# Kernel tuning notes

Hardware: AMD Instinct MI355X
Metric: run time of the kernel (lower is better)

## Reference

```python
import jax, jax.numpy as jnp
import numpy as np

N, K, D = 100000, 16, 128

def setup_inputs() -> dict:
    key = jax.random.key(0)
    k1, k2, k3, k4, k5 = jax.random.split(key, 5)
    s = 1.0 / np.sqrt(D)  # nn.Linear default init scale
    return {
        "h": jax.random.normal(k1, (N, D), dtype=jnp.float32),
        "nbr_idx": jax.random.randint(k2, (N, K), 0, N, dtype=jnp.int64),
        "nbr_w": jax.random.uniform(k3, (N, K), dtype=jnp.float32),
        "w_self": jax.random.uniform(k4, (D, D), minval=-s, maxval=s, dtype=jnp.float32),
        "w_nei": jax.random.uniform(k5, (D, D), minval=-s, maxval=s, dtype=jnp.float32),
        "ln_gamma": jnp.ones((D,), dtype=jnp.float32),
        "ln_beta": jnp.zeros((D,), dtype=jnp.float32),
    }

def layer_norm(x, gamma, beta, eps=1e-5):
    mu = jnp.mean(x, axis=-1, keepdims=True)
    var = jnp.mean(jnp.square(x - mu), axis=-1, keepdims=True)
    return (x - mu) * jax.lax.rsqrt(var + eps) * gamma + beta

def reference(h, nbr_idx, nbr_w, w_self, w_nei, ln_gamma, ln_beta):
    # gather neighbor features: [N, K, D]
    nei = h[nbr_idx]
    # weighted sum over neighbors -> [N, D]
    agg = jnp.einsum('nk,nkd->nd', nbr_w, nei)
    # dual linear (nn.Linear applies x @ W.T) + exact (erf) GELU
    out = jax.nn.gelu(h @ w_self.T + agg @ w_nei.T, approximate=False)
    # dropout is identity at inference; then LayerNorm
    return layer_norm(out, ln_gamma, ln_beta)
```

## Files before the change

kernel.cpp:

```cpp
#include <hip/hip_runtime.h>
#include <hip/hip_bf16.h>
#include <math.h>

#define DFEAT 128
#define KNBR  16
#define NPB   64

typedef __attribute__((ext_vector_type(8))) short short8;
typedef __attribute__((ext_vector_type(4))) float f32x4;
typedef __attribute__((ext_vector_type(2))) unsigned u32x2;
typedef __attribute__((ext_vector_type(4))) unsigned u32x4;

__device__ __forceinline__ unsigned short f2bf(float x) {
    union { float f; unsigned u; } v; v.f = x;
    unsigned r = v.u + 0x7FFFu + ((v.u >> 16) & 1u);
    return (unsigned short)(r >> 16);
}
__device__ __forceinline__ float bf2f(unsigned short u) {
    union { unsigned u; float f; } v; v.u = ((unsigned)u) << 16; return v.f;
}

__global__ __launch_bounds__(256)
void prep_kernel(const float* __restrict__ h,
                 const float* __restrict__ wself,
                 const float* __restrict__ wnei,
                 unsigned short* __restrict__ h16,
                 unsigned short* __restrict__ wcat,
                 unsigned char* __restrict__ h8i,
                 float* __restrict__ sc,
                 int ntot8) {
    const int t = blockIdx.x * 256 + threadIdx.x;
    if (t < 4096) {
        const int base = t * 8;
        const int j = base >> 8;
        const int d0 = base & 255;
        const float* src = (d0 < DFEAT) ? (wself + j * DFEAT + d0)
                                        : (wnei  + j * DFEAT + (d0 - DFEAT));
        f32x4 a = ((const f32x4*)src)[0], b = ((const f32x4*)src)[1];
        short8 o;
        o[0] = f2bf(a[0]); o[1] = f2bf(a[1]); o[2] = f2bf(a[2]); o[3] = f2bf(a[3]);
        o[4] = f2bf(b[0]); o[5] = f2bf(b[1]); o[6] = f2bf(b[2]); o[7] = f2bf(b[3]);
        *(short8*)(wcat + base) = o;
        return;
    }
    const long u = (long)t - 4096;
    if (u >= ntot8) return;
    f32x4 a = __builtin_nontemporal_load((const f32x4*)(h + u * 8));
    f32x4 b = __builtin_nontemporal_load((const f32x4*)(h + u * 8) + 1);
    short8 o;
    o[0] = f2bf(a[0]); o[1] = f2bf(a[1]); o[2] = f2bf(a[2]); o[3] = f2bf(a[3]);
    o[4] = f2bf(b[0]); o[5] = f2bf(b[1]); o[6] = f2bf(b[2]); o[7] = f2bf(b[3]);
    __builtin_nontemporal_store(o, (short8*)(h16 + u * 8));

    if (h8i) {
        float m = 0.f;
        #pragma unroll
        for (int d = 0; d < 4; ++d) { m = fmaxf(m, fabsf(a[d])); m = fmaxf(m, fabsf(b[d])); }
        #pragma unroll
        for (int mk = 1; mk < 16; mk <<= 1) m = fmaxf(m, __shfl_xor(m, mk, 64));
        const float inv = (m > 0.f) ? 127.f / m : 0.f;
        u32x2 q;
        q[0] = ((unsigned)((int)rintf(a[0] * inv) & 255))
             | ((unsigned)((int)rintf(a[1] * inv) & 255) << 8)
             | ((unsigned)((int)rintf(a[2] * inv) & 255) << 16)
             | ((unsigned)((int)rintf(a[3] * inv) & 255) << 24);
        q[1] = ((unsigned)((int)rintf(b[0] * inv) & 255))
             | ((unsigned)((int)rintf(b[1] * inv) & 255) << 8)
             | ((unsigned)((int)rintf(b[2] * inv) & 255) << 16)
             | ((unsigned)((int)rintf(b[3] * inv) & 255) << 24);
        __builtin_nontemporal_store(q, (u32x2*)(h8i + u * 8));
        if ((u & 15) == 0) sc[u >> 4] = m * (1.f / 127.f);
    }
}

template<int MODE>
__global__ __launch_bounds__(256, 4)
void sage_fused_kernel(const float* __restrict__ h,
                       const unsigned short* __restrict__ h16,
                       const unsigned char* __restrict__ h8i,
                       const float* __restrict__ sc,
                       const int* __restrict__ nbr32,
                       const float* __restrict__ nbrw,
                       const unsigned short* __restrict__ wcat,
                       const float* __restrict__ gamma,
                       const float* __restrict__ beta,
                       float* __restrict__ out,
                       int N) {
    __shared__ __align__(16) unsigned short xlds[NPB][256];

    const int tid = threadIdx.x;
    const int nb  = blockIdx.x * NPB;

    const bool idx64 = ((nbr32[1] | nbr32[3] | nbr32[5] | nbr32[7] |
                         nbr32[9] | nbr32[11] | nbr32[13] | nbr32[15]) == 0);

    const int l   = tid & 63;
    const int wvi = tid >> 6;

    if constexpr (MODE == 3) {
        const int q8  = l & 7;
        const int gb2 = l & 56;
        const int i0b = wvi * 16 + (l >> 3) * 2;

        #pragma unroll
        for (int r = 0; r < 2; ++r) {
            const int i = i0b + r;
            int n = nb + i; if (n >= N) n = N - 1;

            const int e0 = n * KNBR + q8;
            const int id0 = nbr32[idx64 ? 2 * e0 : e0];
            const int id1 = nbr32[idx64 ? 2 * (e0 + 8) : (e0 + 8)];
            const float w0 = nbrw[e0]     * sc[id0];
            const float w1 = nbrw[e0 + 8] * sc[id1];

            short8 hv0 = *(const short8*)(h16 + (long)n * DFEAT + q8 * 16);
            short8 hv1 = *(const short8*)(h16 + (long)n * DFEAT + q8 * 16 + 8);
            *(short8*)&xlds[i][((2 * q8)     ^ (i & 7)) * 8] = hv0;
            *(short8*)&xlds[i][((2 * q8 + 1) ^ (i & 7)) * 8] = hv1;

            float acc[16];
            #pragma unroll
            for (int d = 0; d < 16; ++d) acc[d] = 0.f;

            #pragma unroll
            for (int k = 0; k < 16; ++k) {
                const int   ik = __shfl(k < 8 ? id0 : id1, gb2 + (k & 7), 64);
                const float wk = __shfl(k < 8 ? w0  : w1,  gb2 + (k & 7), 64);
                u32x4 nv = *(const u32x4*)(h8i + (long)ik * DFEAT + q8 * 16);
                #pragma unroll
                for (int b = 0; b < 4; ++b) {
                    const unsigned u = nv[b];
                    acc[b * 4 + 0] += wk * (float)(signed char)(u & 0xFF);
                    acc[b * 4 + 1] += wk * (float)(signed char)((u >> 8) & 0xFF);
                    acc[b * 4 + 2] += wk * (float)(signed char)((u >> 16) & 0xFF);
                    acc[b * 4 + 3] += wk * (float)(signed char)(u >> 24);
                }
            }

            short8 ab0, ab1;
            #pragma unroll
            for (int d = 0; d < 8; ++d) { ab0[d] = f2bf(acc[d]); ab1[d] = f2bf(acc[8 + d]); }
            *(short8*)&xlds[i][((16 + 2 * q8)     ^ (i & 7)) * 8] = ab0;
            *(short8*)&xlds[i][((16 + 2 * q8 + 1) ^ (i & 7)) * 8] = ab1;
        }
    } else if constexpr (MODE == 1) {
        const int q  = l & 15;
        const int gb = l & 48;
        const int i0 = wvi * 16 + (l >> 4) * 4;
        #pragma unroll 1
        for (int r = 0; r < 4; ++r) {
            const int i = i0 + r;
            int n = nb + i; if (n >= N) n = N - 1;
            const int e0 = n * KNBR + q;
            int myidx = nbr32[idx64 ? 2 * e0 : e0];
            float myw = nbrw[e0];
            short8 hv = *(const short8*)(h16 + (long)n * DFEAT + q * 8);
            float acc[8] = {0.f,0.f,0.f,0.f,0.f,0.f,0.f,0.f};
            #pragma unroll
            for (int k = 0; k < KNBR; ++k) {
                int ik = __shfl(myidx, gb + k, 64);
                short8 nv = *(const short8*)(h16 + (long)ik * DFEAT + q * 8);
                float wk = __shfl(myw, gb + k, 64);
                #pragma unroll
                for (int d = 0; d < 8; ++d)
                    acc[d] += wk * bf2f((unsigned short)nv[d]);
            }
            *(short8*)&xlds[i][(q ^ (i & 7)) * 8] = hv;
            short8 ab;
            #pragma unroll
            for (int d = 0; d < 8; ++d) ab[d] = f2bf(acc[d]);
            *(short8*)&xlds[i][((16 + q) ^ (i & 7)) * 8] = ab;
        }
    } else {
        const int q  = l & 15;
        const int i0 = wvi * 16 + (l >> 4) * 4;
        #pragma unroll 1
        for (int r = 0; r < 4; ++r) {
            const int i = i0 + r;
            int n = nb + i; if (n >= N) n = N - 1;
            short8 hv;
            float acc[8] = {0.f,0.f,0.f,0.f,0.f,0.f,0.f,0.f};
            const f32x4* hrow = (const f32x4*)(h + (long)n * DFEAT + q * 8);
            f32x4 h0 = hrow[0], h1 = hrow[1];
            hv[0] = f2bf(h0[0]); hv[1] = f2bf(h0[1]); hv[2] = f2bf(h0[2]); hv[3] = f2bf(h0[3]);
            hv[4] = f2bf(h1[0]); hv[5] = f2bf(h1[1]); hv[6] = f2bf(h1[2]); hv[7] = f2bf(h1[3]);
            const int e0 = n * KNBR;
            #pragma unroll 4
            for (int k = 0; k < KNBR; ++k) {
                float w = nbrw[e0 + k];
                int idx = nbr32[idx64 ? 2 * (e0 + k) : (e0 + k)];
                const f32x4* nrow = (const f32x4*)(h + (long)idx * DFEAT + q * 8);
                f32x4 n0 = nrow[0], n1 = nrow[1];
                acc[0] += w * n0[0]; acc[1] += w * n0[1];
                acc[2] += w * n0[2]; acc[3] += w * n0[3];
                acc[4] += w * n1[0]; acc[5] += w * n1[1];
                acc[6] += w * n1[2]; acc[7] += w * n1[3];
            }
            *(short8*)&xlds[i][(q ^ (i & 7)) * 8] = hv;
            short8 ab;
            #pragma unroll
            for (int d = 0; d < 8; ++d) ab[d] = f2bf(acc[d]);
            *(short8*)&xlds[i][((16 + q) ^ (i & 7)) * 8] = ab;
        }
    }
    __syncthreads();

    const int wv  = wvi;
    const int col = l & 15;
    const int kg  = l >> 4;

    f32x4 acc2[4][2];
    #pragma unroll
    for (int s = 0; s < 4; ++s)
        #pragma unroll
        for (int t = 0; t < 2; ++t)
            acc2[s][t] = (f32x4){0.f, 0.f, 0.f, 0.f};

    const unsigned short* wbase0 = wcat + (wv * 32 + col) * 256 + kg * 8;
    const unsigned short* wbase1 = wbase0 + 16 * 256;

    #pragma unroll
    for (int kk = 0; kk < 8; ++kk) {
        short8 b0 = *(const short8*)(wbase0 + kk * 32);
        short8 b1 = *(const short8*)(wbase1 + kk * 32);
        #pragma unroll
        for (int s = 0; s < 4; ++s) {
            const int row = s * 16 + col;
            const int c = (kk * 4 + kg) ^ (row & 7);
            short8 a = *(const short8*)&xlds[row][c * 8];
            acc2[s][0] = __builtin_amdgcn_mfma_f32_16x16x32_bf16(a, b0, acc2[s][0], 0, 0, 0);
            acc2[s][1] = __builtin_amdgcn_mfma_f32_16x16x32_bf16(a, b1, acc2[s][1], 0, 0, 0);
        }
    }

    float y[4][2][4];
    #pragma unroll
    for (int s = 0; s < 4; ++s)
        #pragma unroll
        for (int t = 0; t < 2; ++t)
            #pragma unroll
            for (int r = 0; r < 4; ++r) {
                float x = acc2[s][t][r];
                y[s][t][r] = 0.5f * x * (1.0f + erff(x * 0.70710678118654752f));
            }

    __syncthreads();

    float* lsum = (float*)&xlds[0][0];
    float* lsq  = lsum + 4 * NPB;

    #pragma unroll
    for (int s = 0; s < 4; ++s) {
        f32x4 sm, sq;
        #pragma unroll
        for (int r = 0; r < 4; ++r) {
            float a0 = y[s][0][r], a1 = y[s][1][r];
            sm[r] = a0 + a1;
            sq[r] = a0 * a0 + a1 * a1;
        }
        #pragma unroll
        for (int m = 1; m < 16; m <<= 1) {
            #pragma unroll
            for (int r = 0; r < 4; ++r) {
                sm[r] += __shfl_xor(sm[r], m, 64);
                sq[r] += __shfl_xor(sq[r], m, 64);
            }
        }
        if (col == 0) {
            *(f32x4*)&lsum[wv * NPB + s * 16 + kg * 4] = sm;
            *(f32x4*)&lsq [wv * NPB + s * 16 + kg * 4] = sq;
        }
    }
    __syncthreads();

    const float g0  = gamma[wv * 32 + col];
    const float g1  = gamma[wv * 32 + 16 + col];
    const float be0 = beta [wv * 32 + col];
    const float be1 = beta [wv * 32 + 16 + col];

    #pragma unroll
    for (int s = 0; s < 4; ++s) {
        f32x4 sm = {0.f,0.f,0.f,0.f}, sq = {0.f,0.f,0.f,0.f};
        #pragma unroll
        for (int u = 0; u < 4; ++u) {
            f32x4 a = *(const f32x4*)&lsum[u * NPB + s * 16 + kg * 4];
            f32x4 b = *(const f32x4*)&lsq [u * NPB + s * 16 + kg * 4];
            sm += a; sq += b;
        }
        #pragma unroll
        for (int r = 0; r < 4; ++r) {
            const int i = s * 16 + kg * 4 + r;
            const int n = nb + i;
            if (n < N) {
                float mean = sm[r] * (1.0f / 128.0f);
                float var  = sq[r] * (1.0f / 128.0f) - mean * mean;
                float rstd = rsqrtf(var + 1e-5f);
                long o = (long)n * DFEAT + wv * 32 + col;
                __builtin_nontemporal_store((y[s][0][r] - mean) * rstd * g0 + be0, &out[o]);
                __builtin_nontemporal_store((y[s][1][r] - mean) * rstd * g1 + be1, &out[o + 16]);
            }
        }
    }
}

extern "C" void kernel_launch(void* const* d_in, const int* in_sizes, int n_in,
                              void* d_out, int out_size, void* d_ws, size_t ws_size,
                              hipStream_t stream) {
    const float* h     = (const float*)d_in[0];
    const int*   nbr   = (const int*)  d_in[1];
    const float* nbrw  = (const float*)d_in[2];
    const float* wself = (const float*)d_in[3];
    const float* wnei  = (const float*)d_in[4];
    const float* gamma = (const float*)d_in[5];
    const float* beta  = (const float*)d_in[6];
    const int N = in_sizes[0] / DFEAT;

    unsigned short* wcat = (unsigned short*)d_ws;
    unsigned short* h16  = (unsigned short*)((char*)d_ws + 65536);
    float*          sc   = (float*)((char*)d_ws + 65536 + (size_t)N * DFEAT * 2);
    unsigned char*  h8i  = (unsigned char*)((char*)sc + (size_t)N * 4);
    const size_t need16 = 65536 + (size_t)N * DFEAT * 2;
    const size_t need3  = need16 + (size_t)N * 4 + (size_t)N * DFEAT;

    const int blocks = (N + NPB - 1) / NPB;
    const int ntot8 = N * DFEAT / 8;
    const int pthreads = 4096 + ntot8;

    if (ws_size >= need3) {
        prep_kernel<<<(pthreads + 255) / 256, 256, 0, stream>>>(h, wself, wnei, h16, wcat, h8i, sc, ntot8);
        sage_fused_kernel<3><<<blocks, 256, 0, stream>>>(h, h16, h8i, sc, nbr, nbrw, wcat,
                                                         gamma, beta, (float*)d_out, N);
    } else if (ws_size >= need16) {
        prep_kernel<<<(pthreads + 255) / 256, 256, 0, stream>>>(h, wself, wnei, h16, wcat,
                                                                (unsigned char*)nullptr, (float*)nullptr, ntot8);
        sage_fused_kernel<1><<<blocks, 256, 0, stream>>>(h, h16, (const unsigned char*)nullptr,
                                                         (const float*)nullptr, nbr, nbrw, wcat,
                                                         gamma, beta, (float*)d_out, N);
    } else {
        prep_kernel<<<(4096 + 255) / 256, 256, 0, stream>>>(h, wself, wnei, h16, wcat,
                                                            (unsigned char*)nullptr, (float*)nullptr, 0);
        sage_fused_kernel<0><<<blocks, 256, 0, stream>>>(h, (const unsigned short*)nullptr,
                                                         (const unsigned char*)nullptr,
                                                         (const float*)nullptr, nbr, nbrw, wcat,
                                                         gamma, beta, (float*)d_out, N);
    }
}
```

Baseline: 85.92 us.

## Split int8 neighbor gather into a separate high-occupancy kernel before the GEMM

Moves the int8 neighbor gather and weighted sum out of the fused GEMM kernel into a standalone gather_kernel with launch bounds allowing 8 blocks per CU. The kernel writes a bf16 aggregate buffer, which the fused kernel (new MODE 4) then loads alongside h16. The aim is to hide random-gather latency with more waves in flight than the register- and LDS-heavy fused kernel allows. In exchange it adds an extra launch and a write plus reread of an N×128 bf16 intermediate, and it needs a larger workspace.

```diff
diff --git a/kernel.cpp b/kernel.cpp
--- a/kernel.cpp
+++ b/kernel.cpp
@@ -18,6 +18,9 @@
 }
 __device__ __forceinline__ float bf2f(unsigned short u) {
     union { unsigned u; float f; } v; v.u = ((unsigned)u) << 16; return v.f;
+}
+__device__ __forceinline__ bool detect_idx64(const int* p) {
+    return ((p[1] | p[3] | p[5] | p[7] | p[9] | p[11] | p[13] | p[15]) == 0);
 }
 
 __global__ __launch_bounds__(256)
@@ -73,12 +76,59 @@
     }
 }
 
+__global__ __launch_bounds__(256, 8)
+void gather_kernel(const unsigned char* __restrict__ h8i,
+                   const float* __restrict__ sc,
+                   const int* __restrict__ nbr32,
+                   const float* __restrict__ nbrw,
+                   unsigned short* __restrict__ agg,
+                   int N) {
+    const bool idx64 = detect_idx64(nbr32);
+    const int tid = threadIdx.x;
+    const int q8  = tid & 7;
+    const int gb  = (tid & 63) & 56;
+    const int n   = (blockIdx.x * 256 + tid) >> 3;
+    if (n >= N) return;
+
+    const int e0  = n * KNBR + q8;
+    const int id0 = nbr32[idx64 ? 2 * e0 : e0];
+    const int id1 = nbr32[idx64 ? 2 * (e0 + 8) : (e0 + 8)];
+    const float w0 = nbrw[e0]     * sc[id0];
+    const float w1 = nbrw[e0 + 8] * sc[id1];
+
+    float acc[16];
+    #pragma unroll
+    for (int d = 0; d < 16; ++d) acc[d] = 0.f;
+
+    #pragma unroll
+    for (int k = 0; k < 16; ++k) {
+        const int   ik = __shfl(k < 8 ? id0 : id1, gb + (k & 7), 64);
+        const float wk = __shfl(k < 8 ? w0  : w1,  gb + (k & 7), 64);
+        u32x4 nv = *(const u32x4*)(h8i + (long)ik * DFEAT + q8 * 16);
+        #pragma unroll
+        for (int b = 0; b < 4; ++b) {
+            const unsigned u = nv[b];
+            acc[b * 4 + 0] += wk * (float)(signed char)(u & 0xFF);
+            acc[b * 4 + 1] += wk * (float)(signed char)((u >> 8) & 0xFF);
+            acc[b * 4 + 2] += wk * (float)(signed char)((u >> 16) & 0xFF);
+            acc[b * 4 + 3] += wk * (float)(signed char)(u >> 24);
+        }
+    }
+
+    short8 o0, o1;
+    #pragma unroll
+    for (int d = 0; d < 8; ++d) { o0[d] = f2bf(acc[d]); o1[d] = f2bf(acc[8 + d]); }
+    __builtin_nontemporal_store(o0, (short8*)(agg + (long)n * DFEAT + q8 * 16));
+    __builtin_nontemporal_store(o1, (short8*)(agg + (long)n * DFEAT + q8 * 16 + 8));
+}
+
 template<int MODE>
 __global__ __launch_bounds__(256, 4)
 void sage_fused_kernel(const float* __restrict__ h,
                        const unsigned short* __restrict__ h16,
                        const unsigned char* __restrict__ h8i,
                        const float* __restrict__ sc,
+                       const unsigned short* __restrict__ aggt,
                        const int* __restrict__ nbr32,
                        const float* __restrict__ nbrw,
                        const unsigned short* __restrict__ wcat,
@@ -90,38 +140,42 @@
 
     const int tid = threadIdx.x;
     const int nb  = blockIdx.x * NPB;
-
-    const bool idx64 = ((nbr32[1] | nbr32[3] | nbr32[5] | nbr32[7] |
-                         nbr32[9] | nbr32[11] | nbr32[13] | nbr32[15]) == 0);
-
     const int l   = tid & 63;
     const int wvi = tid >> 6;
 
-    if constexpr (MODE == 3) {
+    if constexpr (MODE == 4) {
+        const int q  = l & 15;
+        const int i0 = wvi * 16 + (l >> 4) * 4;
+        #pragma unroll
+        for (int r = 0; r < 4; ++r) {
+            const int i = i0 + r;
+            int n = nb + i; if (n >= N) n = N - 1;
+            short8 hv = *(const short8*)(h16  + (long)n * DFEAT + q * 8);
+            short8 av = *(const short8*)(aggt + (long)n * DFEAT + q * 8);
+            *(short8*)&xlds[i][(q ^ (i & 7)) * 8] = hv;
+            *(short8*)&xlds[i][((16 + q) ^ (i & 7)) * 8] = av;
+        }
+    } else if constexpr (MODE == 3) {
+        const bool idx64 = detect_idx64(nbr32);
         const int q8  = l & 7;
         const int gb2 = l & 56;
         const int i0b = wvi * 16 + (l >> 3) * 2;
-
         #pragma unroll
         for (int r = 0; r < 2; ++r) {
             const int i = i0b + r;
             int n = nb + i; if (n >= N) n = N - 1;
-
             const int e0 = n * KNBR + q8;
             const int id0 = nbr32[idx64 ? 2 * e0 : e0];
             const int id1 = nbr32[idx64 ? 2 * (e0 + 8) : (e0 + 8)];
             const float w0 = nbrw[e0]     * sc[id0];
             const float w1 = nbrw[e0 + 8] * sc[id1];
-
             short8 hv0 = *(const short8*)(h16 + (long)n * DFEAT + q8 * 16);
             short8 hv1 = *(const short8*)(h16 + (long)n * DFEAT + q8 * 16 + 8);
             *(short8*)&xlds[i][((2 * q8)     ^ (i & 7)) * 8] = hv0;
             *(short8*)&xlds[i][((2 * q8 + 1) ^ (i & 7)) * 8] = hv1;
-
             float acc[16];
             #pragma unroll
             for (int d = 0; d < 16; ++d) acc[d] = 0.f;
-
             #pragma unroll
             for (int k = 0; k < 16; ++k) {
                 const int   ik = __shfl(k < 8 ? id0 : id1, gb2 + (k & 7), 64);
@@ -136,7 +190,6 @@
                     acc[b * 4 + 3] += wk * (float)(signed char)(u >> 24);
                 }
             }
-
             short8 ab0, ab1;
             #pragma unroll
             for (int d = 0; d < 8; ++d) { ab0[d] = f2bf(acc[d]); ab1[d] = f2bf(acc[8 + d]); }
@@ -144,6 +197,7 @@
             *(short8*)&xlds[i][((16 + 2 * q8 + 1) ^ (i & 7)) * 8] = ab1;
         }
     } else if constexpr (MODE == 1) {
+        const bool idx64 = detect_idx64(nbr32);
         const int q  = l & 15;
         const int gb = l & 48;
         const int i0 = wvi * 16 + (l >> 4) * 4;
@@ -172,6 +226,7 @@
             *(short8*)&xlds[i][((16 + q) ^ (i & 7)) * 8] = ab;
         }
     } else {
+        const bool idx64 = detect_idx64(nbr32);
         const int q  = l & 15;
         const int i0 = wvi * 16 + (l >> 4) * 4;
         #pragma unroll 1
@@ -319,29 +374,36 @@
     unsigned short* h16  = (unsigned short*)((char*)d_ws + 65536);
     float*          sc   = (float*)((char*)d_ws + 65536 + (size_t)N * DFEAT * 2);
     unsigned char*  h8i  = (unsigned char*)((char*)sc + (size_t)N * 4);
-    const size_t need16 = 65536 + (size_t)N * DFEAT * 2;
-    const size_t need3  = need16 + (size_t)N * 4 + (size_t)N * DFEAT;
+    unsigned short* aggt = (unsigned short*)(h8i + (size_t)N * DFEAT);
+    const size_t need16  = 65536 + (size_t)N * DFEAT * 2;
+    const size_t need3   = need16 + (size_t)N * 4 + (size_t)N * DFEAT;
+    const size_t need4   = need3 + (size_t)N * DFEAT * 2;
 
     const int blocks = (N + NPB - 1) / NPB;
     const int ntot8 = N * DFEAT / 8;
     const int pthreads = 4096 + ntot8;
 
-    if (ws_size >= need3) {
+    if (ws_size >= need4) {
         prep_kernel<<<(pthreads + 255) / 256, 256, 0, stream>>>(h, wself, wnei, h16, wcat, h8i, sc, ntot8);
-        sage_fused_kernel<3><<<blocks, 256, 0, stream>>>(h, h16, h8i, sc, nbr, nbrw, wcat,
+        gather_kernel<<<((size_t)N * 8 + 255) / 256, 256, 0, stream>>>(h8i, sc, nbr, nbrw, aggt, N);
+        sage_fused_kernel<4><<<blocks, 256, 0, stream>>>(h, h16, h8i, sc, aggt, nbr, nbrw, wcat,
                                                          gamma, beta, (float*)d_out, N);
+    } else if (ws_size >= need3) {
+        prep_kernel<<<(pthreads + 255) / 256, 256, 0, stream>>>(h, wself, wnei, h16, wcat, h8i, sc, ntot8);
+        sage_fused_kernel<3><<<blocks, 256, 0, stream>>>(h, h16, h8i, sc, (const unsigned short*)nullptr,
+                                                         nbr, nbrw, wcat, gamma, beta, (float*)d_out, N);
     } else if (ws_size >= need16) {
         prep_kernel<<<(pthreads + 255) / 256, 256, 0, stream>>>(h, wself, wnei, h16, wcat,
                                                                 (unsigned char*)nullptr, (float*)nullptr, ntot8);
         sage_fused_kernel<1><<<blocks, 256, 0, stream>>>(h, h16, (const unsigned char*)nullptr,
-                                                         (const float*)nullptr, nbr, nbrw, wcat,
-                                                         gamma, beta, (float*)d_out, N);
+                                                         (const float*)nullptr, (const unsigned short*)nullptr,
+                                                         nbr, nbrw, wcat, gamma, beta, (float*)d_out, N);
     } else {
         prep_kernel<<<(4096 + 255) / 256, 256, 0, stream>>>(h, wself, wnei, h16, wcat,
                                                             (unsigned char*)nullptr, (float*)nullptr, 0);
         sage_fused_kernel<0><<<blocks, 256, 0, stream>>>(h, (const unsigned short*)nullptr,
                                                          (const unsigned char*)nullptr,
-                                                         (const float*)nullptr, nbr, nbrw, wcat,
-                                                         gamma, beta, (float*)d_out, N);
-    }
-}
+                                                         (const float*)nullptr, (const unsigned short*)nullptr,
+                                                         nbr, nbrw, wcat, gamma, beta, (float*)d_out, N);
+    }
+}
```

New measurement: 102.2 us. 18.9% more time.

## Shrink fused block to 32 nodes and 2 waves, each wave covering 64 output columns

Applied to the files above, without the earlier changes.

Halves the nodes per block (64 to 32) and the threads per block (256 to 128). Each of the two waves now computes 64 output columns for 32 rows instead of 32 columns for 64 rows, using four weight fragments per k-step. The LayerNorm partial-sum reduction shrinks to two contributions per row. The aim is more, smaller blocks for better occupancy and load balance, at the cost of each block reloading the full weight matrix for fewer rows.

```diff
diff --git a/kernel.cpp b/kernel.cpp
--- a/kernel.cpp
+++ b/kernel.cpp
@@ -4,7 +4,8 @@
 
 #define DFEAT 128
 #define KNBR  16
-#define NPB   64
+#define NPB   32
+#define NTHR  128
 
 typedef __attribute__((ext_vector_type(8))) short short8;
 typedef __attribute__((ext_vector_type(4))) float f32x4;
@@ -18,6 +19,9 @@
 }
 __device__ __forceinline__ float bf2f(unsigned short u) {
     union { unsigned u; float f; } v; v.u = ((unsigned)u) << 16; return v.f;
+}
+__device__ __forceinline__ bool detect_idx64(const int* p) {
+    return ((p[1] | p[3] | p[5] | p[7] | p[9] | p[11] | p[13] | p[15]) == 0);
 }
 
 __global__ __launch_bounds__(256)
@@ -74,7 +78,7 @@
 }
 
 template<int MODE>
-__global__ __launch_bounds__(256, 4)
+__global__ __launch_bounds__(NTHR, 4)
 void sage_fused_kernel(const float* __restrict__ h,
                        const unsigned short* __restrict__ h16,
                        const unsigned char* __restrict__ h8i,
@@ -90,38 +94,30 @@
 
     const int tid = threadIdx.x;
     const int nb  = blockIdx.x * NPB;
-
-    const bool idx64 = ((nbr32[1] | nbr32[3] | nbr32[5] | nbr32[7] |
-                         nbr32[9] | nbr32[11] | nbr32[13] | nbr32[15]) == 0);
-
     const int l   = tid & 63;
     const int wvi = tid >> 6;
 
     if constexpr (MODE == 3) {
+        const bool idx64 = detect_idx64(nbr32);
         const int q8  = l & 7;
         const int gb2 = l & 56;
         const int i0b = wvi * 16 + (l >> 3) * 2;
-
         #pragma unroll
         for (int r = 0; r < 2; ++r) {
             const int i = i0b + r;
             int n = nb + i; if (n >= N) n = N - 1;
-
             const int e0 = n * KNBR + q8;
             const int id0 = nbr32[idx64 ? 2 * e0 : e0];
             const int id1 = nbr32[idx64 ? 2 * (e0 + 8) : (e0 + 8)];
             const float w0 = nbrw[e0]     * sc[id0];
             const float w1 = nbrw[e0 + 8] * sc[id1];
-
             short8 hv0 = *(const short8*)(h16 + (long)n * DFEAT + q8 * 16);
             short8 hv1 = *(const short8*)(h16 + (long)n * DFEAT + q8 * 16 + 8);
             *(short8*)&xlds[i][((2 * q8)     ^ (i & 7)) * 8] = hv0;
             *(short8*)&xlds[i][((2 * q8 + 1) ^ (i & 7)) * 8] = hv1;
-
             float acc[16];
             #pragma unroll
             for (int d = 0; d < 16; ++d) acc[d] = 0.f;
-
             #pragma unroll
             for (int k = 0; k < 16; ++k) {
                 const int   ik = __shfl(k < 8 ? id0 : id1, gb2 + (k & 7), 64);
@@ -136,7 +132,6 @@
                     acc[b * 4 + 3] += wk * (float)(signed char)(u >> 24);
                 }
             }
-
             short8 ab0, ab1;
             #pragma unroll
             for (int d = 0; d < 8; ++d) { ab0[d] = f2bf(acc[d]); ab1[d] = f2bf(acc[8 + d]); }
@@ -144,6 +139,7 @@
             *(short8*)&xlds[i][((16 + 2 * q8 + 1) ^ (i & 7)) * 8] = ab1;
         }
     } else if constexpr (MODE == 1) {
+        const bool idx64 = detect_idx64(nbr32);
         const int q  = l & 15;
         const int gb = l & 48;
         const int i0 = wvi * 16 + (l >> 4) * 4;
@@ -172,6 +168,7 @@
             *(short8*)&xlds[i][((16 + q) ^ (i & 7)) * 8] = ab;
         }
     } else {
+        const bool idx64 = detect_idx64(nbr32);
         const int q  = l & 15;
         const int i0 = wvi * 16 + (l >> 4) * 4;
         #pragma unroll 1
@@ -209,35 +206,38 @@
     const int col = l & 15;
     const int kg  = l >> 4;
 
-    f32x4 acc2[4][2];
-    #pragma unroll
-    for (int s = 0; s < 4; ++s)
-        #pragma unroll
-        for (int t = 0; t < 2; ++t)
+    f32x4 acc2[2][4];
+    #pragma unroll
+    for (int s = 0; s < 2; ++s)
+        #pragma unroll
+        for (int t = 0; t < 4; ++t)
             acc2[s][t] = (f32x4){0.f, 0.f, 0.f, 0.f};
 
-    const unsigned short* wbase0 = wcat + (wv * 32 + col) * 256 + kg * 8;
-    const unsigned short* wbase1 = wbase0 + 16 * 256;
+    const unsigned short* wb0 = wcat + (wv * 64 + col) * 256 + kg * 8;
 
     #pragma unroll
     for (int kk = 0; kk < 8; ++kk) {
-        short8 b0 = *(const short8*)(wbase0 + kk * 32);
-        short8 b1 = *(const short8*)(wbase1 + kk * 32);
-        #pragma unroll
-        for (int s = 0; s < 4; ++s) {
+        short8 bt0 = *(const short8*)(wb0 + kk * 32);
+        short8 bt1 = *(const short8*)(wb0 + 16 * 256 + kk * 32);
+        short8 bt2 = *(const short8*)(wb0 + 32 * 256 + kk * 32);
+        short8 bt3 = *(const short8*)(wb0 + 48 * 256 + kk * 32);
+        #pragma unroll
+        for (int s = 0; s < 2; ++s) {
             const int row = s * 16 + col;
             const int c = (kk * 4 + kg) ^ (row & 7);
             short8 a = *(const short8*)&xlds[row][c * 8];
-            acc2[s][0] = __builtin_amdgcn_mfma_f32_16x16x32_bf16(a, b0, acc2[s][0], 0, 0, 0);
-            acc2[s][1] = __builtin_amdgcn_mfma_f32_16x16x32_bf16(a, b1, acc2[s][1], 0, 0, 0);
-        }
-    }
-
-    float y[4][2][4];
-    #pragma unroll
-    for (int s = 0; s < 4; ++s)
-        #pragma unroll
-        for (int t = 0; t < 2; ++t)
+            acc2[s][0] = __builtin_amdgcn_mfma_f32_16x16x32_bf16(a, bt0, acc2[s][0], 0, 0, 0);
+            acc2[s][1] = __builtin_amdgcn_mfma_f32_16x16x32_bf16(a, bt1, acc2[s][1], 0, 0, 0);
+            acc2[s][2] = __builtin_amdgcn_mfma_f32_16x16x32_bf16(a, bt2, acc2[s][2], 0, 0, 0);
+            acc2[s][3] = __builtin_amdgcn_mfma_f32_16x16x32_bf16(a, bt3, acc2[s][3], 0, 0, 0);
+        }
+    }
+
+    float y[2][4][4];
+    #pragma unroll
+    for (int s = 0; s < 2; ++s)
+        #pragma unroll
+        for (int t = 0; t < 4; ++t)
             #pragma unroll
             for (int r = 0; r < 4; ++r) {
                 float x = acc2[s][t][r];
@@ -247,16 +247,16 @@
     __syncthreads();
 
     float* lsum = (float*)&xlds[0][0];
-    float* lsq  = lsum + 4 * NPB;
-
-    #pragma unroll
-    for (int s = 0; s < 4; ++s) {
+    float* lsq  = lsum + 2 * NPB;
+
+    #pragma unroll
+    for (int s = 0; s < 2; ++s) {
         f32x4 sm, sq;
         #pragma unroll
         for (int r = 0; r < 4; ++r) {
-            float a0 = y[s][0][r], a1 = y[s][1][r];
-            sm[r] = a0 + a1;
-            sq[r] = a0 * a0 + a1 * a1;
+            float a0 = y[s][0][r], a1 = y[s][1][r], a2 = y[s][2][r], a3 = y[s][3][r];
+            sm[r] = (a0 + a1) + (a2 + a3);
+            sq[r] = (a0 * a0 + a1 * a1) + (a2 * a2 + a3 * a3);
         }
         #pragma unroll
         for (int m = 1; m < 16; m <<= 1) {
@@ -273,19 +273,22 @@
     }
     __syncthreads();
 
-    const float g0  = gamma[wv * 32 + col];
-    const float g1  = gamma[wv * 32 + 16 + col];
-    const float be0 = beta [wv * 32 + col];
-    const float be1 = beta [wv * 32 + 16 + col];
-
-    #pragma unroll
-    for (int s = 0; s < 4; ++s) {
-        f32x4 sm = {0.f,0.f,0.f,0.f}, sq = {0.f,0.f,0.f,0.f};
-        #pragma unroll
-        for (int u = 0; u < 4; ++u) {
-            f32x4 a = *(const f32x4*)&lsum[u * NPB + s * 16 + kg * 4];
-            f32x4 b = *(const f32x4*)&lsq [u * NPB + s * 16 + kg * 4];
-            sm += a; sq += b;
+    float g[4], be[4];
+    #pragma unroll
+    for (int t = 0; t < 4; ++t) {
+        g[t]  = gamma[wv * 64 + t * 16 + col];
+        be[t] = beta [wv * 64 + t * 16 + col];
+    }
+
+    #pragma unroll
+    for (int s = 0; s < 2; ++s) {
+        f32x4 sm, sq;
+        {
+            f32x4 a0 = *(const f32x4*)&lsum[0 * NPB + s * 16 + kg * 4];
+            f32x4 a1 = *(const f32x4*)&lsum[1 * NPB + s * 16 + kg * 4];
+            f32x4 b0 = *(const f32x4*)&lsq [0 * NPB + s * 16 + kg * 4];
+            f32x4 b1 = *(const f32x4*)&lsq [1 * NPB + s * 16 + kg * 4];
+            sm = a0 + a1; sq = b0 + b1;
         }
         #pragma unroll
         for (int r = 0; r < 4; ++r) {
@@ -295,9 +298,11 @@
                 float mean = sm[r] * (1.0f / 128.0f);
                 float var  = sq[r] * (1.0f / 128.0f) - mean * mean;
                 float rstd = rsqrtf(var + 1e-5f);
-                long o = (long)n * DFEAT + wv * 32 + col;
-                __builtin_nontemporal_store((y[s][0][r] - mean) * rstd * g0 + be0, &out[o]);
-                __builtin_nontemporal_store((y[s][1][r] - mean) * rstd * g1 + be1, &out[o + 16]);
+                long o = (long)n * DFEAT + wv * 64 + col;
+                #pragma unroll
+                for (int t = 0; t < 4; ++t)
+                    __builtin_nontemporal_store((y[s][t][r] - mean) * rstd * g[t] + be[t],
+                                                &out[o + t * 16]);
             }
         }
     }
@@ -328,20 +333,20 @@
 
     if (ws_size >= need3) {
         prep_kernel<<<(pthreads + 255) / 256, 256, 0, stream>>>(h, wself, wnei, h16, wcat, h8i, sc, ntot8);
-        sage_fused_kernel<3><<<blocks, 256, 0, stream>>>(h, h16, h8i, sc, nbr, nbrw, wcat,
-                                                         gamma, beta, (float*)d_out, N);
+        sage_fused_kernel<3><<<blocks, NTHR, 0, stream>>>(h, h16, h8i, sc, nbr, nbrw, wcat,
+                                                          gamma, beta, (float*)d_out, N);
     } else if (ws_size >= need16) {
         prep_kernel<<<(pthreads + 255) / 256, 256, 0, stream>>>(h, wself, wnei, h16, wcat,
                                                                 (unsigned char*)nullptr, (float*)nullptr, ntot8);
-        sage_fused_kernel<1><<<blocks, 256, 0, stream>>>(h, h16, (const unsigned char*)nullptr,
-                                                         (const float*)nullptr, nbr, nbrw, wcat,
-                                                         gamma, beta, (float*)d_out, N);
+        sage_fused_kernel<1><<<blocks, NTHR, 0, stream>>>(h, h16, (const unsigned char*)nullptr,
+                                                          (const float*)nullptr, nbr, nbrw, wcat,
+                                                          gamma, beta, (float*)d_out, N);
     } else {
         prep_kernel<<<(4096 + 255) / 256, 256, 0, stream>>>(h, wself, wnei, h16, wcat,
                                                             (unsigned char*)nullptr, (float*)nullptr, 0);
-        sage_fused_kernel<0><<<blocks, 256, 0, stream>>>(h, (const unsigned short*)nullptr,
-                                                         (const unsigned char*)nullptr,
-                                                         (const float*)nullptr, nbr, nbrw, wcat,
-                                                         gamma, beta, (float*)d_out, N);
-    }
-}
+        sage_fused_kernel<0><<<blocks, NTHR, 0, stream>>>(h, (const unsigned short*)nullptr,
+                                                          (const unsigned char*)nullptr,
+                                                          (const float*)nullptr, nbr, nbrw, wcat,
+                                                          gamma, beta, (float*)d_out, N);
+    }
+}
```

Result: slower. 89.16 us (+3.8%).
